# Kernel tuning notes

Measured on AMD Instinct MI355X. Metric: run time of the kernel, lower is better.

Reference implementation:

```python
import jax, jax.numpy as jnp
from jax import lax
import numpy as np

# ITA requantization params (from init_kwargs)
MQ, SQ = 16384, 8
MK, SK = 16384, 8
MV, SV = 16384, 8
MA, SA = 5, 12
MAV, SAV = 1, 8
MO, SO = 256, 7
NUM_HEADS = 6


def requantize(x, mult, shift, add=0):
    # x * mult, floor-div by 2**shift, add, clamp to int8 range (values kept in float32)
    return jnp.clip(jnp.floor(x * mult / (2.0 ** shift)) + add, -128.0, 127.0)


def ita_softmax(x):
    # x: [B, h, S, Skv] float32 with integer values in [-128, 127]
    B, h, S, Skv = x.shape
    width, bits = 16, 8
    eps_max = 32.0 * bits / (2 ** bits)  # range_scale * bits / 2**bits = 1.0
    groups = Skv // width
    x3 = x.reshape(B * h, S, Skv).astype(jnp.int32)
    # [groups, BH, S, width] for streaming scan over key chunks
    chunks = x3.reshape(B * h, S, groups, width).transpose(2, 0, 1, 3)

    def step(carry, chunk):
        exp_partial_sum, global_max = carry
        current_max = chunk.max(axis=-1)
        update = current_max > global_max
        max_shift = jnp.floor((current_max - global_max).astype(jnp.float32) * eps_max + 0.5).astype(jnp.int32)
        shift_sum = jnp.where(update, max_shift, 0)
        global_max = jnp.where(update, current_max, global_max)
        diff = global_max[..., None] - chunk  # >= 0
        shift = jnp.floor(diff.astype(jnp.float32) * eps_max + 0.5).astype(jnp.int32)
        # 2**bits >> shift  (256 >> shift; any shift >= 9 yields 0, clamp to keep shift defined)
        exp_sum = jnp.sum(jnp.right_shift(jnp.int32(256), jnp.minimum(shift, 31)), axis=-1).astype(jnp.int32)
        exp_partial_sum = jnp.right_shift(exp_partial_sum, jnp.minimum(shift_sum, 31)) + exp_sum
        return (exp_partial_sum, global_max), None

    init = (jnp.zeros((B * h, S), jnp.int32), jnp.full((B * h, S), -128, jnp.int32))
    (exp_partial_sum, global_max), _ = lax.scan(step, init, chunks)

    # (2**bits - 1) * 2**bits = 65280
    inv = jnp.floor(65280.0 / exp_partial_sum.astype(jnp.float32)).astype(jnp.int32)
    diff = global_max[..., None] - x3  # >= 0
    shift = jnp.floor(diff.astype(jnp.float32) * eps_max + 0.5).astype(jnp.int32)
    res = jnp.right_shift(inv[..., None], jnp.minimum(shift, 31)).astype(jnp.uint8)
    return res.reshape(B, h, S, Skv)


def setup_inputs() -> dict:
    key = jax.random.key(0)
    ks = jax.random.split(key, 9)
    B, N, D = 4, 2048, 384
    scale = 1.0 / np.sqrt(D)
    return {
        "x": jax.random.normal(ks[0], (B, N, D), jnp.float32),
        "wq": jax.random.normal(ks[1], (D, D), jnp.float32) * scale,
        "bq": jnp.zeros((D,), jnp.float32),
        "wk": jax.random.normal(ks[2], (D, D), jnp.float32) * scale,
        "bk": jnp.zeros((D,), jnp.float32),
        "wv": jax.random.normal(ks[3], (D, D), jnp.float32) * scale,
        "bv": jnp.zeros((D,), jnp.float32),
        "wo": jax.random.normal(ks[4], (D, D), jnp.float32) * scale,
        "bo": jnp.zeros((D,), jnp.float32),
        "H": 64,
        "W": 32,
    }


def reference(x, wq, bq, wk, bk, wv, bv, wo, bo, H, W):
    B, N, _ = x.shape
    h = NUM_HEADS
    hd = wq.shape[0] // h

    Q = requantize(x @ wq.T + bq, MQ, SQ)
    K = requantize(x @ wk.T + bk, MK, SK)
    V = requantize(x @ wv.T + bv, MV, SV)

    Qr = Q.reshape(B, N, h, hd).transpose(0, 2, 1, 3)  # [B,h,N,hd]
    Kr = K.reshape(B, N, h, hd).transpose(0, 2, 1, 3)
    Vr = V.reshape(B, N, h, hd).transpose(0, 2, 1, 3)

    logits = requantize(jnp.einsum('bhqd,bhkd->bhqk', Qr, Kr), MA, SA)
    attn = ita_softmax(logits)  # uint8 [B,h,N,N]
    ctx = requantize(jnp.einsum('bhqk,bhkd->bhqd', attn.astype(jnp.float32), Vr), MAV, SAV)
    ctx = ctx.transpose(0, 2, 1, 3).reshape(B, N, h * hd)
    out = requantize(ctx @ wo.T + bo, MO, SO)
    return out
```

## Files before the change

kernel.cpp:

```cpp
#include <hip/hip_runtime.h>
#include <stdint.h>

#define NB 4
#define NN 2048
#define ND 384
#define NH 6
#define HD 64
#define ROWS (NB * NN)

typedef int v4i __attribute__((ext_vector_type(4)));
typedef float v4f __attribute__((ext_vector_type(4)));
typedef _Float16 half_t;
typedef half_t v8h __attribute__((ext_vector_type(8)));

__global__ __launch_bounds__(256) void qkv_gemm_kernel(
    const float* __restrict__ X,
    const float* __restrict__ Wq, const float* __restrict__ Wk, const float* __restrict__ Wv,
    const float* __restrict__ Bq, const float* __restrict__ Bk, const float* __restrict__ Bv,
    int8_t* __restrict__ Q8, int8_t* __restrict__ K8, int8_t* __restrict__ V8T,
    int* __restrict__ CS)
{
    __shared__ float As[16][132];
    __shared__ float Bs[16][76];
    __shared__ int lcol[64];

    const int t = threadIdx.x;
    const int row0 = blockIdx.x * 128;
    const int c0g = blockIdx.y * 64;
    const int m = c0g / ND;
    const int cl0 = c0g - m * ND;
    const float* W = (m == 0) ? Wq : (m == 1) ? Wk : Wv;
    const float* Bi = (m == 0) ? Bq : (m == 1) ? Bk : Bv;

    const int tx = t & 15;
    const int ty = t >> 4;
    const int lr = t >> 1;
    const int kh = (t & 1) * 8;
    const int rb = t >> 2;
    const int kb = (t & 3) * 4;

    float acc[8][4];
#pragma unroll
    for (int i = 0; i < 8; i++)
#pragma unroll
        for (int j = 0; j < 4; j++) acc[i][j] = 0.f;

    const float* xrow = X + (size_t)(row0 + lr) * ND + kh;
    const float* wrow = W + (size_t)(cl0 + rb) * ND + kb;

    for (int k0 = 0; k0 < ND; k0 += 16) {
        float4 a0 = *(const float4*)(xrow + k0);
        float4 a1 = *(const float4*)(xrow + k0 + 4);
        float4 b0 = *(const float4*)(wrow + k0);
        As[kh + 0][lr] = a0.x; As[kh + 1][lr] = a0.y; As[kh + 2][lr] = a0.z; As[kh + 3][lr] = a0.w;
        As[kh + 4][lr] = a1.x; As[kh + 5][lr] = a1.y; As[kh + 6][lr] = a1.z; As[kh + 7][lr] = a1.w;
        Bs[kb + 0][rb] = b0.x; Bs[kb + 1][rb] = b0.y; Bs[kb + 2][rb] = b0.z; Bs[kb + 3][rb] = b0.w;
        __syncthreads();
#pragma unroll
        for (int kk = 0; kk < 16; kk++) {
            float4 av0 = *(const float4*)&As[kk][ty * 8];
            float4 av1 = *(const float4*)&As[kk][ty * 8 + 4];
            float4 bv  = *(const float4*)&Bs[kk][tx * 4];
            float a[8] = {av0.x, av0.y, av0.z, av0.w, av1.x, av1.y, av1.z, av1.w};
            float b[4] = {bv.x, bv.y, bv.z, bv.w};
#pragma unroll
            for (int i = 0; i < 8; i++)
#pragma unroll
                for (int j = 0; j < 4; j++)
                    acc[i][j] += a[i] * b[j];
        }
        __syncthreads();
    }

    const int bidx = row0 >> 11;
    const int n0 = row0 & 2047;
    const int head = cl0 >> 6;
    if (m == 2) {
        if (t < 64) lcol[t] = 0;
        __syncthreads();
#pragma unroll
        for (int j = 0; j < 4; j++) {
            const int dim = tx * 4 + j;
            const float bias = Bi[cl0 + dim];
            int s = 0;
            uint32_t w[2] = {0u, 0u};
#pragma unroll
            for (int i = 0; i < 8; i++) {
                float v = acc[i][j] + bias;
                int qv = (int)floorf(v * 64.0f);
                qv = max(-128, min(127, qv));
                s += qv;
                w[i >> 2] |= (uint32_t)(qv & 255) << (8 * (i & 3));
            }
            uint32_t* dst = (uint32_t*)(V8T + (((size_t)(bidx * NH + head) * HD + dim) * NN
                                              + n0 + ty * 8));
            dst[0] = w[0];
            dst[1] = w[1];
            atomicAdd(&lcol[dim], s);
        }
        __syncthreads();
        if (t < 64)
            atomicAdd(&CS[(bidx * NH + head) * 64 + t], lcol[t]);
    } else {
        int8_t* Out = (m == 0) ? Q8 : K8;
#pragma unroll
        for (int i = 0; i < 8; i++) {
            const int n = n0 + ty * 8 + i;
            uint32_t w = 0;
#pragma unroll
            for (int j = 0; j < 4; j++) {
                float v = acc[i][j] + Bi[cl0 + tx * 4 + j];
                int qv = (int)floorf(v * 64.0f);
                qv = max(-128, min(127, qv));
                w |= (uint32_t)(qv & 255) << (8 * j);
            }
            *(uint32_t*)(Out + (((size_t)(bidx * NH + head) * NN) + n) * HD + tx * 4) = w;
        }
    }
}

__global__ __launch_bounds__(256, 4) void attn_kernel(
    const int8_t* __restrict__ Q8, const int8_t* __restrict__ K8,
    const int8_t* __restrict__ V8T, const int* __restrict__ colsum,
    int8_t* __restrict__ CTX8)
{
    __shared__ int Lp[128 * 68];
    __shared__ int gmaxw[128 * 4];
    __shared__ int esumw[128 * 8];

    const int t = threadIdx.x;
    const int wid = t >> 6;
    const int lane = t & 63;
    const int quad = lane >> 4;
    const int l15 = lane & 15;
    const int bh = blockIdx.y;
    const int q0 = blockIdx.x * 16;
    const size_t base = (size_t)bh * NN * HD;
    const v4i zero = {0, 0, 0, 0};

    v4i afrag = *(const v4i*)(Q8 + base + (size_t)(q0 + l15) * HD + quad * 16);
    {
        const int8_t* kp = K8 + base + (size_t)(wid * 32 * 16 + l15) * HD + quad * 16;
        v4i bfrag = *(const v4i*)kp;
        for (int kt = wid * 32; kt < wid * 32 + 32; ++kt) {
            v4i cur = bfrag;
            kp += 16 * HD;
            bfrag = *(const v4i*)kp;
            v4i d = __builtin_amdgcn_mfma_i32_16x16x64_i8(afrag, cur, zero, 0, 0, 0);
            int e[4];
#pragma unroll
            for (int r = 0; r < 4; ++r) {
                int lg = (d[r] * 5) >> 12;
                e[r] = min(127, max(-128, lg));
            }
            int p01 = __builtin_amdgcn_perm(e[1], e[0], 0x00000400);
            int p23 = __builtin_amdgcn_perm(e[3], e[2], 0x00000400);
            Lp[kt * 68 + quad * 16 + l15] = __builtin_amdgcn_perm(p23, p01, 0x05040100);
        }
    }
    __syncthreads();

    int wb[2][16];
#pragma unroll
    for (int it = 0; it < 2; ++it) {
        const int task = t + it * 256;
        const int g = task & 127, qq = task >> 7;
        const int* p = &Lp[g * 68 + qq * 16];
#pragma unroll
        for (int a = 0; a < 4; ++a) {
            v4i v = *(const v4i*)&p[a * 4];
            wb[it][a * 4 + 0] = v.x; wb[it][a * 4 + 1] = v.y;
            wb[it][a * 4 + 2] = v.z; wb[it][a * 4 + 3] = v.w;
        }
        int mx[4];
#pragma unroll
        for (int b = 0; b < 4; ++b) {
            int m = INT_MIN;
#pragma unroll
            for (int j = 0; j < 16; ++j)
                m = max(m, (int)((unsigned)wb[it][j] << (8 * (3 - b))));
            mx[b] = m;
        }
        int p01 = __builtin_amdgcn_perm(mx[1], mx[0], 0x00000703);
        int p23 = __builtin_amdgcn_perm(mx[3], mx[2], 0x00000703);
        gmaxw[g * 4 + qq] = __builtin_amdgcn_perm(p23, p01, 0x05040100);
    }
    __syncthreads();

    if (t < 16) {
        const int wq = t >> 2, bq = 8 * (t & 3);
        int8_t* gb = (int8_t*)gmaxw;
        int m = -128;
        for (int g = 0; g < 128; ++g) {
            int x = (int)(int8_t)(gmaxw[g * 4 + wq] >> bq);
            m = max(m, x);
            gb[g * 16 + t] = (int8_t)m;
        }
    }
    __syncthreads();

#pragma unroll
    for (int it = 0; it < 2; ++it) {
        const int task = t + it * 256;
        const int g = task & 127, qq = task >> 7;
        const int pw = gmaxw[g * 4 + qq];
        uint32_t sp[2] = {0u, 0u};
#pragma unroll
        for (int b = 0; b < 4; ++b) {
            const int M = (int)(int8_t)(pw >> (8 * b));
            const int cb = 8 - M;
            int s = 0;
#pragma unroll
            for (int j = 0; j < 16; ++j) {
                int x = (int)(int8_t)(wb[it][j] >> (8 * b));
                int tt = x + cb;
                s += (tt >= 0) ? (1 << tt) : 0;
            }
            sp[b >> 1] |= (uint32_t)s << (16 * (b & 1));
        }
        *(int2*)&esumw[g * 8 + qq * 2] = make_int2((int)sp[0], (int)sp[1]);
    }
    __syncthreads();

    if (t < 16) {
        const int8_t* gb = (const int8_t*)gmaxw;
        const uint16_t* eb = (const uint16_t*)esumw;
        int E = 0, Mp = -128;
        for (int g = 0; g < 128; ++g) {
            int m = (int)gb[g * 16 + t];
            int d = m - Mp; if (d > 31) d = 31;
            E = (E >> d) + (int)eb[g * 16 + t];
            Mp = m;
        }
        Lp[t * 68 + 64] = 65280 / E;
        Lp[t * 68 + 65] = Mp;
    }
    __syncthreads();

    const int inv_l = Lp[l15 * 68 + 64];
    const int c24 = 24 - Lp[l15 * 68 + 65];
    const int sh8 = 8 * (l15 & 3);
    v4i accs[4] = {zero, zero, zero, zero};
    const int8_t* vtb = V8T + base;

    v4i bf[4];
    {
        const int koff0 = wid * 8 * 64 + quad * 16;
#pragma unroll
        for (int dtb = 0; dtb < 4; ++dtb)
            bf[dtb] = *(const v4i*)(vtb + (size_t)(dtb * 16 + l15) * NN + koff0);
    }
    for (int kc = wid * 8; kc < wid * 8 + 8; ++kc) {
        const int* lp = &Lp[(kc * 4 + quad) * 68 + (l15 >> 2) * 16];
        v4i w4[4];
#pragma unroll
        for (int r = 0; r < 4; ++r) w4[r] = *(const v4i*)&lp[4 * r];

        v4i b0 = bf[0], b1 = bf[1], b2 = bf[2], b3 = bf[3];
        const int koffn = (kc + 1) * 64 + quad * 16;
#pragma unroll
        for (int dtb = 0; dtb < 4; ++dtb)
            bf[dtb] = *(const v4i*)(vtb + (size_t)(dtb * 16 + l15) * NN + koffn);

        v4i a;
#pragma unroll
        for (int r = 0; r < 4; ++r) {
            int u[4];
#pragma unroll
            for (int c = 0; c < 4; ++c) {
                int x = (int)(int8_t)(w4[r][c] >> sh8);
                int t1 = x + c24;
                t1 = (t1 < 0) ? 0 : t1;
                u[c] = (int)((unsigned)inv_l << t1);
            }
            int p01 = __builtin_amdgcn_perm(u[1], u[0], 0x00000703);
            int p23 = __builtin_amdgcn_perm(u[3], u[2], 0x00000703);
            a[r] = __builtin_amdgcn_perm(p23, p01, 0x05040100) ^ (int)0x80808080u;
        }
        accs[0] = __builtin_amdgcn_mfma_i32_16x16x64_i8(a, b0, accs[0], 0, 0, 0);
        accs[1] = __builtin_amdgcn_mfma_i32_16x16x64_i8(a, b1, accs[1], 0, 0, 0);
        accs[2] = __builtin_amdgcn_mfma_i32_16x16x64_i8(a, b2, accs[2], 0, 0, 0);
        accs[3] = __builtin_amdgcn_mfma_i32_16x16x64_i8(a, b3, accs[3], 0, 0, 0);
    }
    __syncthreads();

    if (wid > 0) {
#pragma unroll
        for (int dt = 0; dt < 4; ++dt)
#pragma unroll
            for (int r = 0; r < 4; ++r)
                Lp[(dt * 4 + r) * 192 + (wid - 1) * 64 + lane] = accs[dt][r];
    }
    __syncthreads();
    if (wid == 0) {
        const int bb = bh / NH, hh = bh % NH;
        const int* cs = &colsum[bh * 64];
#pragma unroll
        for (int dt = 0; dt < 4; ++dt) {
            const int dcol = dt * 16 + l15;
            const int corr = cs[dcol] << 7;
#pragma unroll
            for (int r = 0; r < 4; ++r) {
                const int i = dt * 4 + r;
                int val = accs[dt][r]
                        + Lp[i * 192 + 0 * 64 + lane]
                        + Lp[i * 192 + 1 * 64 + lane]
                        + Lp[i * 192 + 2 * 64 + lane];
                const int q = q0 + quad * 4 + r;
                val = (val + corr) >> 8;
                val = min(127, max(-128, val));
                CTX8[((size_t)(bb * NN + q)) * ND + hh * HD + dcol] = (int8_t)val;
            }
        }
    }
}

__global__ __launch_bounds__(256) void out_gemm_kernel(
    const int8_t* __restrict__ CTX8, const float* __restrict__ Wo,
    const float* __restrict__ Bo, float* __restrict__ out)
{
    __shared__ __attribute__((aligned(16))) half_t AH[64 * 40];
    __shared__ __attribute__((aligned(16))) half_t BH[64 * 40];
    __shared__ __attribute__((aligned(16))) half_t BL[64 * 40];

    const int t = threadIdx.x;
    const int wid = t >> 6;
    const int lane = t & 63;
    const int quad = lane >> 4;
    const int l15 = lane & 15;
    const int row0 = blockIdx.x * 64;
    const int c0 = blockIdx.y * 64;

    const int arow = t >> 2;
    const int akb = (t & 3) * 8;
    const int8_t* ap = CTX8 + (size_t)(row0 + arow) * ND + akb;
    const float* wp = Wo + (size_t)(c0 + arow) * ND + akb;

    v4f accH[4], accL[4];
#pragma unroll
    for (int ct = 0; ct < 4; ct++) { accH[ct] = (v4f)0.0f; accL[ct] = (v4f)0.0f; }

    for (int k0 = 0; k0 < ND; k0 += 32) {
        int2 a8 = *(const int2*)(ap + k0);
        float4 w0 = *(const float4*)(wp + k0);
        float4 w1 = *(const float4*)(wp + k0 + 4);
        float wsrc[8] = {w0.x, w0.y, w0.z, w0.w, w1.x, w1.y, w1.z, w1.w};

        __syncthreads();
        v8h av, wh8, wl8;
#pragma unroll
        for (int u = 0; u < 4; u++) {
            av[u]     = (half_t)(float)(int)(int8_t)((a8.x >> (8 * u)) & 0xFF);
            av[4 + u] = (half_t)(float)(int)(int8_t)((a8.y >> (8 * u)) & 0xFF);
        }
#pragma unroll
        for (int u = 0; u < 8; u++) {
            float x = wsrc[u];
            half_t h = (half_t)x;
            wh8[u] = h;
            wl8[u] = (half_t)((x - (float)h) * 2048.0f);
        }
        *(v8h*)&AH[arow * 40 + akb] = av;
        *(v8h*)&BH[arow * 40 + akb] = wh8;
        *(v8h*)&BL[arow * 40 + akb] = wl8;
        __syncthreads();

        v8h af = *(const v8h*)&AH[(wid * 16 + l15) * 40 + quad * 8];
#pragma unroll
        for (int ct = 0; ct < 4; ct++) {
            v8h bh8 = *(const v8h*)&BH[(ct * 16 + l15) * 40 + quad * 8];
            v8h bl8 = *(const v8h*)&BL[(ct * 16 + l15) * 40 + quad * 8];
            accH[ct] = __builtin_amdgcn_mfma_f32_16x16x32_f16(af, bh8, accH[ct], 0, 0, 0);
            accL[ct] = __builtin_amdgcn_mfma_f32_16x16x32_f16(af, bl8, accL[ct], 0, 0, 0);
        }
    }

    const float inv2048 = 4.8828125e-4f;
#pragma unroll
    for (int ct = 0; ct < 4; ct++) {
        const int c = c0 + ct * 16 + l15;
        const float bias = Bo[c];
#pragma unroll
        for (int r = 0; r < 4; r++) {
            const int row = row0 + wid * 16 + quad * 4 + r;
            float v = accH[ct][r] + accL[ct][r] * inv2048 + bias;
            float rq = floorf(v * 2.0f);
            rq = fminf(fmaxf(rq, -128.0f), 127.0f);
            out[(size_t)row * ND + c] = rq;
        }
    }
}

extern "C" void kernel_launch(void* const* d_in, const int* in_sizes, int n_in,
                              void* d_out, int out_size, void* d_ws, size_t ws_size,
                              hipStream_t stream)
{
    const float* x  = (const float*)d_in[0];
    const float* wq = (const float*)d_in[1];
    const float* bq = (const float*)d_in[2];
    const float* wk = (const float*)d_in[3];
    const float* bk = (const float*)d_in[4];
    const float* wv = (const float*)d_in[5];
    const float* bv = (const float*)d_in[6];
    const float* wo = (const float*)d_in[7];
    const float* bo = (const float*)d_in[8];
    float* out = (float*)d_out;

    const size_t MAT = (size_t)ROWS * ND;
    int8_t* Q8  = (int8_t*)d_ws;
    int8_t* K8  = Q8 + MAT;
    int8_t* V8T = K8 + MAT;
    int8_t* C8  = V8T + MAT;
    int*    CS  = (int*)(C8 + MAT);

    hipMemsetAsync(CS, 0, (size_t)NB * NH * 64 * sizeof(int), stream);
    qkv_gemm_kernel<<<dim3(ROWS / 128, 1152 / 64), 256, 0, stream>>>(
        x, wq, wk, wv, bq, bk, bv, Q8, K8, V8T, CS);
    attn_kernel<<<dim3(NN / 16, NB * NH), 256, 0, stream>>>(Q8, K8, V8T, CS, C8);
    out_gemm_kernel<<<dim3(ROWS / 64, ND / 64), 256, 0, stream>>>(C8, wo, bo, out);
}
```

Before: 277.7 us.

## Retile QKV GEMM to 64x96 tiles with register-prefetched global loads

The QKV projection GEMM now uses 64-thread blocks, each computing a 64x96 output tile with an 8x12 register accumulator per thread, instead of 256-thread blocks on 128x64 tiles. Global loads for the next k-slice are issued into registers before the compute on the current slice, to overlap memory latency with FMA work. The epilogue handles output tiles that span head boundaries. The cost is far fewer threads per block and higher register pressure, which could reduce occupancy and latency hiding.

```diff
diff --git a/kernel.cpp b/kernel.cpp
--- a/kernel.cpp
+++ b/kernel.cpp
@@ -13,60 +13,81 @@
 typedef _Float16 half_t;
 typedef half_t v8h __attribute__((ext_vector_type(8)));
 
-__global__ __launch_bounds__(256) void qkv_gemm_kernel(
+__global__ __launch_bounds__(64, 2) void qkv_gemm_kernel(
     const float* __restrict__ X,
     const float* __restrict__ Wq, const float* __restrict__ Wk, const float* __restrict__ Wv,
     const float* __restrict__ Bq, const float* __restrict__ Bk, const float* __restrict__ Bv,
     int8_t* __restrict__ Q8, int8_t* __restrict__ K8, int8_t* __restrict__ V8T,
     int* __restrict__ CS)
 {
-    __shared__ float As[16][132];
-    __shared__ float Bs[16][76];
-    __shared__ int lcol[64];
+    __shared__ __attribute__((aligned(16))) float As[16][68];
+    __shared__ __attribute__((aligned(16))) float Bs[16][100];
+    __shared__ int lcol[96];
 
     const int t = threadIdx.x;
-    const int row0 = blockIdx.x * 128;
-    const int c0g = blockIdx.y * 64;
-    const int m = c0g / ND;
-    const int cl0 = c0g - m * ND;
+    const int row0 = blockIdx.x * 64;
+    const int cg = blockIdx.y * 96;
+    const int m = cg / 384;
+    const int cl0 = cg - m * 384;
     const float* W = (m == 0) ? Wq : (m == 1) ? Wk : Wv;
     const float* Bi = (m == 0) ? Bq : (m == 1) ? Bk : Bv;
 
-    const int tx = t & 15;
-    const int ty = t >> 4;
-    const int lr = t >> 1;
-    const int kh = (t & 1) * 8;
-    const int rb = t >> 2;
-    const int kb = (t & 3) * 4;
-
-    float acc[8][4];
-#pragma unroll
-    for (int i = 0; i < 8; i++)
-#pragma unroll
-        for (int j = 0; j < 4; j++) acc[i][j] = 0.f;
-
-    const float* xrow = X + (size_t)(row0 + lr) * ND + kh;
-    const float* wrow = W + (size_t)(cl0 + rb) * ND + kb;
+    const int ty = t >> 3;
+    const int tx = t & 7;
+    const int lr = t >> 2;
+    const int kc = (t & 3) * 4;
+
+    float acc[8][12];
+#pragma unroll
+    for (int i = 0; i < 8; ++i)
+#pragma unroll
+        for (int j = 0; j < 12; ++j) acc[i][j] = 0.f;
+
+    const float* xp = X + (size_t)(row0 + lr) * ND + kc;
+    const float* wp = W + (size_t)(cl0 + lr) * ND + kc;
+
+    float4 ar[4], br[6];
+#pragma unroll
+    for (int i = 0; i < 4; ++i) ar[i] = *(const float4*)(xp + (size_t)(16 * i) * ND);
+#pragma unroll
+    for (int i = 0; i < 6; ++i) br[i] = *(const float4*)(wp + (size_t)(16 * i) * ND);
 
     for (int k0 = 0; k0 < ND; k0 += 16) {
-        float4 a0 = *(const float4*)(xrow + k0);
-        float4 a1 = *(const float4*)(xrow + k0 + 4);
-        float4 b0 = *(const float4*)(wrow + k0);
-        As[kh + 0][lr] = a0.x; As[kh + 1][lr] = a0.y; As[kh + 2][lr] = a0.z; As[kh + 3][lr] = a0.w;
-        As[kh + 4][lr] = a1.x; As[kh + 5][lr] = a1.y; As[kh + 6][lr] = a1.z; As[kh + 7][lr] = a1.w;
-        Bs[kb + 0][rb] = b0.x; Bs[kb + 1][rb] = b0.y; Bs[kb + 2][rb] = b0.z; Bs[kb + 3][rb] = b0.w;
-        __syncthreads();
-#pragma unroll
-        for (int kk = 0; kk < 16; kk++) {
-            float4 av0 = *(const float4*)&As[kk][ty * 8];
-            float4 av1 = *(const float4*)&As[kk][ty * 8 + 4];
-            float4 bv  = *(const float4*)&Bs[kk][tx * 4];
-            float a[8] = {av0.x, av0.y, av0.z, av0.w, av1.x, av1.y, av1.z, av1.w};
-            float b[4] = {bv.x, bv.y, bv.z, bv.w};
-#pragma unroll
-            for (int i = 0; i < 8; i++)
-#pragma unroll
-                for (int j = 0; j < 4; j++)
+#pragma unroll
+        for (int i = 0; i < 4; ++i) {
+            As[kc + 0][lr + 16 * i] = ar[i].x; As[kc + 1][lr + 16 * i] = ar[i].y;
+            As[kc + 2][lr + 16 * i] = ar[i].z; As[kc + 3][lr + 16 * i] = ar[i].w;
+        }
+#pragma unroll
+        for (int i = 0; i < 6; ++i) {
+            Bs[kc + 0][lr + 16 * i] = br[i].x; Bs[kc + 1][lr + 16 * i] = br[i].y;
+            Bs[kc + 2][lr + 16 * i] = br[i].z; Bs[kc + 3][lr + 16 * i] = br[i].w;
+        }
+        __syncthreads();
+
+        if (k0 + 16 < ND) {
+#pragma unroll
+            for (int i = 0; i < 4; ++i)
+                ar[i] = *(const float4*)(xp + (k0 + 16) + (size_t)(16 * i) * ND);
+#pragma unroll
+            for (int i = 0; i < 6; ++i)
+                br[i] = *(const float4*)(wp + (k0 + 16) + (size_t)(16 * i) * ND);
+        }
+
+#pragma unroll
+        for (int kk = 0; kk < 16; ++kk) {
+            float4 a0 = *(const float4*)&As[kk][ty * 8];
+            float4 a1 = *(const float4*)&As[kk][ty * 8 + 4];
+            float4 b0 = *(const float4*)&Bs[kk][tx * 4];
+            float4 b1 = *(const float4*)&Bs[kk][tx * 4 + 32];
+            float4 b2 = *(const float4*)&Bs[kk][tx * 4 + 64];
+            float a[8] = {a0.x, a0.y, a0.z, a0.w, a1.x, a1.y, a1.z, a1.w};
+            float b[12] = {b0.x, b0.y, b0.z, b0.w, b1.x, b1.y, b1.z, b1.w,
+                           b2.x, b2.y, b2.z, b2.w};
+#pragma unroll
+            for (int i = 0; i < 8; ++i)
+#pragma unroll
+                for (int j = 0; j < 12; ++j)
                     acc[i][j] += a[i] * b[j];
         }
         __syncthreads();
@@ -74,47 +95,67 @@
 
     const int bidx = row0 >> 11;
     const int n0 = row0 & 2047;
-    const int head = cl0 >> 6;
+
     if (m == 2) {
-        if (t < 64) lcol[t] = 0;
-        __syncthreads();
-#pragma unroll
-        for (int j = 0; j < 4; j++) {
-            const int dim = tx * 4 + j;
-            const float bias = Bi[cl0 + dim];
-            int s = 0;
-            uint32_t w[2] = {0u, 0u};
-#pragma unroll
-            for (int i = 0; i < 8; i++) {
-                float v = acc[i][j] + bias;
-                int qv = (int)floorf(v * 64.0f);
-                qv = max(-128, min(127, qv));
-                s += qv;
-                w[i >> 2] |= (uint32_t)(qv & 255) << (8 * (i & 3));
-            }
-            uint32_t* dst = (uint32_t*)(V8T + (((size_t)(bidx * NH + head) * HD + dim) * NN
-                                              + n0 + ty * 8));
-            dst[0] = w[0];
-            dst[1] = w[1];
-            atomicAdd(&lcol[dim], s);
-        }
-        __syncthreads();
-        if (t < 64)
-            atomicAdd(&CS[(bidx * NH + head) * 64 + t], lcol[t]);
+        lcol[t] = 0;
+        if (t < 32) lcol[64 + t] = 0;
+        __syncthreads();
+#pragma unroll
+        for (int g = 0; g < 3; ++g) {
+#pragma unroll
+            for (int j = 0; j < 4; ++j) {
+                const int c = g * 32 + tx * 4 + j;
+                const int col = cl0 + c;
+                const int head = col >> 6, d = col & 63;
+                const float bias = Bi[col];
+                int s = 0;
+                uint32_t w[2] = {0u, 0u};
+#pragma unroll
+                for (int i = 0; i < 8; ++i) {
+                    float v = acc[i][g * 4 + j] + bias;
+                    int qv = (int)floorf(v * 64.0f);
+                    qv = max(-128, min(127, qv));
+                    s += qv;
+                    w[i >> 2] |= (uint32_t)(qv & 255) << (8 * (i & 3));
+                }
+                uint32_t* dst = (uint32_t*)(V8T + ((size_t)(bidx * NH + head) * HD + d) * NN
+                                            + n0 + ty * 8);
+                dst[0] = w[0];
+                dst[1] = w[1];
+                atomicAdd(&lcol[c], s);
+            }
+        }
+        __syncthreads();
+        {
+            int col = cl0 + t;
+            atomicAdd(&CS[(bidx * NH + (col >> 6)) * 64 + (col & 63)], lcol[t]);
+            if (t < 32) {
+                col = cl0 + 64 + t;
+                atomicAdd(&CS[(bidx * NH + (col >> 6)) * 64 + (col & 63)], lcol[64 + t]);
+            }
+        }
     } else {
         int8_t* Out = (m == 0) ? Q8 : K8;
 #pragma unroll
-        for (int i = 0; i < 8; i++) {
-            const int n = n0 + ty * 8 + i;
-            uint32_t w = 0;
-#pragma unroll
-            for (int j = 0; j < 4; j++) {
-                float v = acc[i][j] + Bi[cl0 + tx * 4 + j];
-                int qv = (int)floorf(v * 64.0f);
-                qv = max(-128, min(127, qv));
-                w |= (uint32_t)(qv & 255) << (8 * j);
-            }
-            *(uint32_t*)(Out + (((size_t)(bidx * NH + head) * NN) + n) * HD + tx * 4) = w;
+        for (int g = 0; g < 3; ++g) {
+            const int colbase = cl0 + g * 32 + tx * 4;
+            const int head = colbase >> 6, d = colbase & 63;
+            const float bias[4] = {Bi[colbase], Bi[colbase + 1],
+                                   Bi[colbase + 2], Bi[colbase + 3]};
+            int8_t* op = Out + ((size_t)(bidx * NH + head) * NN) * HD + d;
+#pragma unroll
+            for (int i = 0; i < 8; ++i) {
+                const int n = n0 + ty * 8 + i;
+                uint32_t w = 0;
+#pragma unroll
+                for (int j = 0; j < 4; ++j) {
+                    float v = acc[i][g * 4 + j] + bias[j];
+                    int qv = (int)floorf(v * 64.0f);
+                    qv = max(-128, min(127, qv));
+                    w |= (uint32_t)(qv & 255) << (8 * j);
+                }
+                *(uint32_t*)(op + (size_t)n * HD) = w;
+            }
         }
     }
 }
@@ -414,7 +455,7 @@
     int*    CS  = (int*)(C8 + MAT);
 
     hipMemsetAsync(CS, 0, (size_t)NB * NH * 64 * sizeof(int), stream);
-    qkv_gemm_kernel<<<dim3(ROWS / 128, 1152 / 64), 256, 0, stream>>>(
+    qkv_gemm_kernel<<<dim3(ROWS / 64, 12), 64, 0, stream>>>(
         x, wq, wk, wv, bq, bk, bv, Q8, K8, V8T, CS);
     attn_kernel<<<dim3(NN / 16, NB * NH), 256, 0, stream>>>(Q8, K8, V8T, CS, C8);
     out_gemm_kernel<<<dim3(ROWS / 64, ND / 64), 256, 0, stream>>>(C8, wo, bo, out);
```

Measured after the change: 340.9 us. +22.8%, slower.

## Restructure QKV GEMM to read weights via wave-uniform scalar loads with register prefetch

Applied to the files above, without the earlier changes.

The QKV projection kernel now uses 384-thread blocks with 96-column tiles. Each wave owns 16 output columns and reads weights straight from global memory using a wave-uniform (readfirstlane) address, so they can become scalar loads and the shared-memory B tile is dropped. X tiles are prefetched into registers for the next k-step. The V epilogue replaces shared-memory atomics with wave shuffles plus one global atomic per column. The costs are heavy scalar-load traffic, larger register arrays, and fewer blocks.

```diff
diff --git a/kernel.cpp b/kernel.cpp
--- a/kernel.cpp
+++ b/kernel.cpp
@@ -13,108 +13,115 @@
 typedef _Float16 half_t;
 typedef half_t v8h __attribute__((ext_vector_type(8)));
 
-__global__ __launch_bounds__(256) void qkv_gemm_kernel(
+__global__ __launch_bounds__(384, 5) void qkv_gemm_kernel(
     const float* __restrict__ X,
     const float* __restrict__ Wq, const float* __restrict__ Wk, const float* __restrict__ Wv,
     const float* __restrict__ Bq, const float* __restrict__ Bk, const float* __restrict__ Bv,
     int8_t* __restrict__ Q8, int8_t* __restrict__ K8, int8_t* __restrict__ V8T,
     int* __restrict__ CS)
 {
-    __shared__ float As[16][132];
-    __shared__ float Bs[16][76];
-    __shared__ int lcol[64];
+    __shared__ __attribute__((aligned(16))) float As[16][132];
 
     const int t = threadIdx.x;
+    const int lane = t & 63;
+    const int wid = t >> 6;
     const int row0 = blockIdx.x * 128;
-    const int c0g = blockIdx.y * 64;
-    const int m = c0g / ND;
-    const int cl0 = c0g - m * ND;
+    const int cg = blockIdx.y * 96;
+    const int m = cg / 384;
+    const int cl0 = cg - m * 384;
     const float* W = (m == 0) ? Wq : (m == 1) ? Wk : Wv;
     const float* Bi = (m == 0) ? Bq : (m == 1) ? Bk : Bv;
 
-    const int tx = t & 15;
-    const int ty = t >> 4;
-    const int lr = t >> 1;
-    const int kh = (t & 1) * 8;
-    const int rb = t >> 2;
-    const int kb = (t & 3) * 4;
-
-    float acc[8][4];
-#pragma unroll
-    for (int i = 0; i < 8; i++)
-#pragma unroll
-        for (int j = 0; j < 4; j++) acc[i][j] = 0.f;
-
-    const float* xrow = X + (size_t)(row0 + lr) * ND + kh;
-    const float* wrow = W + (size_t)(cl0 + rb) * ND + kb;
+    const int cw = cl0 + (__builtin_amdgcn_readfirstlane(wid) << 4);
+    const float* wb = W + (size_t)cw * ND;
+
+    const int sr = t >> 2;
+    const int kc = (t & 3) * 4;
+    const float* xp0 = X + (size_t)(row0 + sr) * ND + kc;
+    const float* xp1 = X + (size_t)(row0 + sr + 64) * ND + kc;
+
+    float acc0[16], acc1[16];
+#pragma unroll
+    for (int c = 0; c < 16; ++c) { acc0[c] = 0.f; acc1[c] = 0.f; }
+
+    float4 ar0, ar1;
+    if (t < 256) { ar0 = *(const float4*)xp0; ar1 = *(const float4*)xp1; }
 
     for (int k0 = 0; k0 < ND; k0 += 16) {
-        float4 a0 = *(const float4*)(xrow + k0);
-        float4 a1 = *(const float4*)(xrow + k0 + 4);
-        float4 b0 = *(const float4*)(wrow + k0);
-        As[kh + 0][lr] = a0.x; As[kh + 1][lr] = a0.y; As[kh + 2][lr] = a0.z; As[kh + 3][lr] = a0.w;
-        As[kh + 4][lr] = a1.x; As[kh + 5][lr] = a1.y; As[kh + 6][lr] = a1.z; As[kh + 7][lr] = a1.w;
-        Bs[kb + 0][rb] = b0.x; Bs[kb + 1][rb] = b0.y; Bs[kb + 2][rb] = b0.z; Bs[kb + 3][rb] = b0.w;
+        if (t < 256) {
+            As[kc + 0][sr] = ar0.x; As[kc + 1][sr] = ar0.y;
+            As[kc + 2][sr] = ar0.z; As[kc + 3][sr] = ar0.w;
+            As[kc + 0][sr + 64] = ar1.x; As[kc + 1][sr + 64] = ar1.y;
+            As[kc + 2][sr + 64] = ar1.z; As[kc + 3][sr + 64] = ar1.w;
+        }
         __syncthreads();
-#pragma unroll
-        for (int kk = 0; kk < 16; kk++) {
-            float4 av0 = *(const float4*)&As[kk][ty * 8];
-            float4 av1 = *(const float4*)&As[kk][ty * 8 + 4];
-            float4 bv  = *(const float4*)&Bs[kk][tx * 4];
-            float a[8] = {av0.x, av0.y, av0.z, av0.w, av1.x, av1.y, av1.z, av1.w};
-            float b[4] = {bv.x, bv.y, bv.z, bv.w};
-#pragma unroll
-            for (int i = 0; i < 8; i++)
-#pragma unroll
-                for (int j = 0; j < 4; j++)
-                    acc[i][j] += a[i] * b[j];
+        if (t < 256 && k0 + 16 < ND) {
+            ar0 = *(const float4*)(xp0 + k0 + 16);
+            ar1 = *(const float4*)(xp1 + k0 + 16);
+        }
+        const float* wk0 = wb + k0;
+#pragma unroll
+        for (int kk = 0; kk < 16; ++kk) {
+            float2 a = *(const float2*)&As[kk][2 * lane];
+#pragma unroll
+            for (int c = 0; c < 16; ++c) {
+                float b = wk0[c * ND + kk];
+                acc0[c] = fmaf(a.x, b, acc0[c]);
+                acc1[c] = fmaf(a.y, b, acc1[c]);
+            }
         }
         __syncthreads();
     }
 
     const int bidx = row0 >> 11;
     const int n0 = row0 & 2047;
-    const int head = cl0 >> 6;
-    if (m == 2) {
-        if (t < 64) lcol[t] = 0;
-        __syncthreads();
-#pragma unroll
-        for (int j = 0; j < 4; j++) {
-            const int dim = tx * 4 + j;
-            const float bias = Bi[cl0 + dim];
-            int s = 0;
-            uint32_t w[2] = {0u, 0u};
-#pragma unroll
-            for (int i = 0; i < 8; i++) {
-                float v = acc[i][j] + bias;
-                int qv = (int)floorf(v * 64.0f);
-                qv = max(-128, min(127, qv));
-                s += qv;
-                w[i >> 2] |= (uint32_t)(qv & 255) << (8 * (i & 3));
-            }
-            uint32_t* dst = (uint32_t*)(V8T + (((size_t)(bidx * NH + head) * HD + dim) * NN
-                                              + n0 + ty * 8));
-            dst[0] = w[0];
-            dst[1] = w[1];
-            atomicAdd(&lcol[dim], s);
-        }
-        __syncthreads();
-        if (t < 64)
-            atomicAdd(&CS[(bidx * NH + head) * 64 + t], lcol[t]);
+    const int head = cw >> 6;
+    const int d0 = cw & 63;
+
+    if (m != 2) {
+        int8_t* Out = (m == 0) ? Q8 : K8;
+#pragma unroll
+        for (int r = 0; r < 2; ++r) {
+            const int n = n0 + 2 * lane + r;
+            const float* accp = r ? acc1 : acc0;
+            uint32_t w[4];
+#pragma unroll
+            for (int j4 = 0; j4 < 4; ++j4) {
+                uint32_t w_ = 0;
+#pragma unroll
+                for (int j = 0; j < 4; ++j) {
+                    const int c = j4 * 4 + j;
+                    float v = accp[c] + Bi[cw + c];
+                    int qv = (int)floorf(v * 64.0f);
+                    qv = max(-128, min(127, qv));
+                    w_ |= (uint32_t)(qv & 255) << (8 * j);
+                }
+                w[j4] = w_;
+            }
+            *(int4*)(Out + (((size_t)(bidx * NH + head) * NN) + n) * HD + d0) =
+                make_int4((int)w[0], (int)w[1], (int)w[2], (int)w[3]);
+        }
     } else {
-        int8_t* Out = (m == 0) ? Q8 : K8;
-#pragma unroll
-        for (int i = 0; i < 8; i++) {
-            const int n = n0 + ty * 8 + i;
-            uint32_t w = 0;
-#pragma unroll
-            for (int j = 0; j < 4; j++) {
-                float v = acc[i][j] + Bi[cl0 + tx * 4 + j];
-                int qv = (int)floorf(v * 64.0f);
-                qv = max(-128, min(127, qv));
-                w |= (uint32_t)(qv & 255) << (8 * j);
-            }
-            *(uint32_t*)(Out + (((size_t)(bidx * NH + head) * NN) + n) * HD + tx * 4) = w;
+        int8_t* vb = V8T + ((size_t)(bidx * NH + head) * HD + d0) * NN + n0 + 2 * lane;
+        int csum[16];
+#pragma unroll
+        for (int c = 0; c < 16; ++c) {
+            const float bias = Bi[cw + c];
+            float v0 = acc0[c] + bias;
+            float v1 = acc1[c] + bias;
+            int q0v = (int)floorf(v0 * 64.0f); q0v = max(-128, min(127, q0v));
+            int q1v = (int)floorf(v1 * 64.0f); q1v = max(-128, min(127, q1v));
+            csum[c] = q0v + q1v;
+            *(uint16_t*)(vb + (size_t)c * NN) =
+                (uint16_t)((q0v & 255) | ((q1v & 255) << 8));
+        }
+#pragma unroll
+        for (int c = 0; c < 16; ++c) {
+            int s = csum[c];
+#pragma unroll
+            for (int off = 32; off; off >>= 1) s += __shfl_xor(s, off, 64);
+            if (lane == 0)
+                atomicAdd(&CS[(bidx * NH + head) * 64 + d0 + c], s);
         }
     }
 }
@@ -414,7 +421,7 @@
     int*    CS  = (int*)(C8 + MAT);
 
     hipMemsetAsync(CS, 0, (size_t)NB * NH * 64 * sizeof(int), stream);
-    qkv_gemm_kernel<<<dim3(ROWS / 128, 1152 / 64), 256, 0, stream>>>(
+    qkv_gemm_kernel<<<dim3(ROWS / 128, 12), 384, 0, stream>>>(
         x, wq, wk, wv, bq, bk, bv, Q8, K8, V8T, CS);
     attn_kernel<<<dim3(NN / 16, NB * NH), 256, 0, stream>>>(Q8, K8, V8T, CS, C8);
     out_gemm_kernel<<<dim3(ROWS / 64, ND / 64), 256, 0, stream>>>(C8, wo, bo, out);
```

After: 731.9 us. 164% more time.
